# Optimization experiments

Measured on AMD Instinct MI355X. Metric: run time of the kernel, lower is better.

Reference implementation:

```python
import jax, jax.numpy as jnp
import numpy as np

S, N, L, B = 200000, 250000, 64, 64


def setup_inputs() -> dict:
    key = jax.random.key(0)
    k = jax.random.split(key, 7)
    return {
        "We_m": jax.random.normal(k[0], (S, L), jnp.float32) * 0.02,
        "be_m": jax.random.normal(k[1], (L,), jnp.float32) * 0.02,
        "Wd_m": jax.random.normal(k[2], (L, S), jnp.float32) * 0.02,
        "bd_m": jax.random.normal(k[3], (S,), jnp.float32) * 0.02,
        "x": jax.random.normal(k[4], (B, N), jnp.float32),
        "nn_n": jax.random.randint(k[5], (N,), 0, S),  # nearest master node for each new node
        "nn_m": jax.random.randint(k[6], (S,), 0, N),  # nearest new node for each master node
    }


def _reshape_weights(We_m, be_m, Wd_m, bd_m, nn_n, nn_m):
    # Vectorized equivalent of GFN_AE.reshape_weights(expand=True, agglomerate=True,
    # update_master=False, eval mode).
    s, l = We_m.shape
    n = nn_n.shape[0]
    # Expand: new node pt_n is "added" iff nn_m[nn_n[pt_n]] != pt_n.
    added = (nn_m[nn_n] != jnp.arange(n)).astype(We_m.dtype)  # [N]
    # Sequential We_i[pt_m] *= c/(c+1) collapses to division by (c_m + 1),
    # c_m = number of added new nodes whose nearest master node is m.
    c_m = jax.ops.segment_sum(added, nn_n, num_segments=s)  # [S]
    We_s = We_m / (c_m + 1.0)[:, None]  # scaled master encoder rows
    # Appended row i (for added node pt_n, src m = nn_n[pt_n]) equals We_s[m],
    # Wd column / bd entry copied from m; its nn_m_ext entry is pt_n itself.
    # Agglomerate: We_n sums contributors, Wd_n/bd_n take the running mean (= plain mean).
    We_n = jax.ops.segment_sum(We_s, nn_m, num_segments=n) + added[:, None] * We_s[nn_n]
    WdT = Wd_m.T  # [S, L]
    cnt = jax.ops.segment_sum(jnp.ones((s,), We_m.dtype), nn_m, num_segments=n) + added
    denom = jnp.maximum(cnt, 1.0)
    Wd_n = ((jax.ops.segment_sum(WdT, nn_m, num_segments=n) + added[:, None] * WdT[nn_n]) / denom[:, None]).T  # [L, N]
    bd_n = (jax.ops.segment_sum(bd_m, nn_m, num_segments=n) + added * bd_m[nn_n]) / denom  # [N]
    return We_n, Wd_n, bd_n


def reference(We_m, be_m, Wd_m, bd_m, x, nn_n, nn_m):
    We_n, Wd_n, bd_n = _reshape_weights(We_m, be_m, Wd_m, bd_m, nn_n, nn_m)
    z = x @ We_n + be_m            # encode: [B, N] x [N, L]
    out = z @ Wd_n + bd_n          # decode: [B, L] x [L, N]
    return out
```

## Files before the change

### kernel.cpp

```cpp
#include <hip/hip_runtime.h>

constexpr int S_ = 200000;
constexpr int N_ = 250000;

constexpr int NCHUNK = (N_ + 63) / 64;
constexpr int FUSE_BLOCKS = (NCHUNK + 1) / 2;
constexpr int DEC_BLOCKS = NCHUNK;

constexpr int EMASK = 0x3FFFF;

typedef __attribute__((ext_vector_type(8))) short bf16x8;
typedef __attribute__((ext_vector_type(4))) float f32x4;
typedef __attribute__((ext_vector_type(8))) unsigned short us8;

__global__ void k_added_counts(const int* __restrict__ nn_n, const int* __restrict__ nn_m,
                               int* __restrict__ added, int* __restrict__ c_m,
                               int* __restrict__ ecnt) {
    int i = blockIdx.x * 256 + threadIdx.x;
    if (i < N_) {
        int m = nn_n[i];
        int a = (nn_m[m] != i) ? 1 : 0;
        added[i] = a;
        if (a) {
            atomicAdd(&c_m[m], 1);
            atomicAdd(&ecnt[i], 1);
        }
    }
    if (i < S_) {
        atomicAdd(&ecnt[nn_m[i]], 1);
    }
}

__global__ void k_scan_blocksum(const int* __restrict__ ecnt, int* __restrict__ bsum) {
    __shared__ int sd[256];
    int b = blockIdx.x, t = threadIdx.x;
    int base = b * 1024 + t * 4;
    int s = 0;
#pragma unroll
    for (int k = 0; k < 4; k++) { int idx = base + k; if (idx < N_) s += ecnt[idx]; }
    sd[t] = s;
    __syncthreads();
    for (int off = 128; off > 0; off >>= 1) {
        if (t < off) sd[t] += sd[t + off];
        __syncthreads();
    }
    if (t == 0) bsum[b] = sd[0];
}

__global__ void k_scan_apply(const int* __restrict__ ecnt, const int* __restrict__ bsum,
                             int* __restrict__ offs) {
    __shared__ int sd[256];
    __shared__ int sp[256];
    int b = blockIdx.x, t = threadIdx.x;
    sp[t] = (t < b) ? bsum[t] : 0;
    __syncthreads();
    for (int off = 128; off > 0; off >>= 1) {
        if (t < off) sp[t] += sp[t + off];
        __syncthreads();
    }
    int prev = sp[0];

    int base = b * 1024 + t * 4;
    int v[4]; int s = 0;
#pragma unroll
    for (int k = 0; k < 4; k++) { int idx = base + k; v[k] = (idx < N_) ? ecnt[idx] : 0; s += v[k]; }
    sd[t] = s;
    __syncthreads();
    for (int off = 1; off < 256; off <<= 1) {
        int xv = (t >= off) ? sd[t - off] : 0;
        __syncthreads();
        sd[t] += xv;
        __syncthreads();
    }
    int run = prev + sd[t] - s;
#pragma unroll
    for (int k = 0; k < 4; k++) {
        int idx = base + k;
        if (idx < N_) offs[idx] = run;
        run += v[k];
    }
}

__global__ void k_fill(const int* __restrict__ nn_m, const int* __restrict__ nn_n,
                       const int* __restrict__ added, const int* __restrict__ offs,
                       const int* __restrict__ c_m,
                       int* __restrict__ fill, int* __restrict__ elist) {
    int i = blockIdx.x * 256 + threadIdx.x;
    if (i < S_) {
        int j = nn_m[i];
        int p = atomicAdd(&fill[j], 1);
        elist[offs[j] + p] = i | (c_m[i] << 18);
    }
    if (i < N_ && added[i]) {
        int m = nn_n[i];
        int p = atomicAdd(&fill[i], 1);
        elist[offs[i] + p] = m | (c_m[m] << 18);
    }
}

__global__ __launch_bounds__(256) void k_wenc(
        const float* __restrict__ x, const float* __restrict__ We_m,
        const int* __restrict__ ecnt, const int* __restrict__ offs,
        const int* __restrict__ elist, float* __restrict__ zp2) {
    __shared__ unsigned short sw[8192];
    int t = threadIdx.x;
    int lane = t & 63;
    int wv = __builtin_amdgcn_readfirstlane(t >> 6);
    int mrow = lane & 15;
    int kq = lane >> 4;
    int ct = lane >> 4, l15 = lane & 15;
    const float* xbase = x + (size_t)(wv * 16 + mrow) * N_ + kq * 8;
    f32x4 acc[4];
#pragma unroll
    for (int i = 0; i < 4; i++) acc[i] = (f32x4){0.f, 0.f, 0.f, 0.f};

    for (int cc = 0; cc < 2; cc++) {
        int chk = blockIdx.x * 2 + cc;
        if (chk >= NCHUNK) break;
        int n0 = chk * 64;

        __syncthreads();
        int jb = n0 + wv * 16;
        int c[16], o[16];
        float ag[16];
#pragma unroll
        for (int u = 0; u < 16; u++) {
            int j = jb + u;
            bool v = (j < N_);
            c[u] = v ? __builtin_amdgcn_readfirstlane(ecnt[j]) : 0;
            o[u] = v ? __builtin_amdgcn_readfirstlane(offs[j]) : 0;
            ag[u] = 0.f;
        }
        int cmax = 0;
#pragma unroll
        for (int u = 0; u < 16; u++) cmax = max(cmax, c[u]);
        if (cmax > 0) {
            int e[16];
#pragma unroll
            for (int u = 0; u < 16; u++)
                e[u] = __builtin_amdgcn_readfirstlane(elist[o[u]]);
            for (int q = 0; q < cmax; q++) {
                int en[16];
#pragma unroll
                for (int u = 0; u < 16; u++) {
                    int cl = max(c[u] - 1, 0);
                    int p = o[u] + min(q + 1, cl);
                    en[u] = __builtin_amdgcn_readfirstlane(elist[p]);
                }
                float row[16];
#pragma unroll
                for (int u = 0; u < 16; u++) {
                    int mmu = (q < c[u]) ? (e[u] & EMASK) : 0;
                    const float* ap = We_m + (size_t)mmu * 64 + lane;
                    asm volatile("global_load_dword %0, %1, off"
                                 : "=v"(row[u]) : "v"(ap));
                }
                asm volatile("s_waitcnt vmcnt(0)");
                __builtin_amdgcn_sched_barrier(0);
#pragma unroll
                for (int u = 0; u < 16; u++) {
                    float r = __builtin_amdgcn_rcpf((float)((e[u] >> 18) + 1));
                    float sc = (q < c[u]) ? r : 0.0f;
                    ag[u] += row[u] * sc;
                }
#pragma unroll
                for (int u = 0; u < 16; u++) e[u] = en[u];
            }
        }
        us8 h0, l0, h1, l1;
#pragma unroll
        for (int s = 0; s < 8; s++) {
            float v0 = ag[s];
            unsigned u0 = __float_as_uint(v0);
            h0[s] = (unsigned short)(u0 >> 16);
            float r0 = v0 - __uint_as_float(u0 & 0xffff0000u);
            l0[s] = (unsigned short)(__float_as_uint(r0) >> 16);
            float v1 = ag[8 + s];
            unsigned u1 = __float_as_uint(v1);
            h1[s] = (unsigned short)(u1 >> 16);
            float r1 = v1 - __uint_as_float(u1 & 0xffff0000u);
            l1[s] = (unsigned short)(__float_as_uint(r1) >> 16);
        }
        int kq2a = (wv & 1) * 2;
        int sH = wv >> 1;
        int base0 = sH * 4096 + ct * 1024 + (l15 + 16 * kq2a) * 8;
        int base1 = base0 + 128;
        *(us8*)&sw[base0]       = h0;
        *(us8*)&sw[base0 + 512] = l0;
        *(us8*)&sw[base1]       = h1;
        *(us8*)&sw[base1 + 512] = l1;
        __syncthreads();

#pragma unroll
        for (int s = 0; s < 2; s++) {
            float av[8];
            if (n0 + s * 32 + kq * 8 + 8 <= N_) {
                float4 a0 = *(const float4*)(xbase + n0 + s * 32);
                float4 a1 = *(const float4*)(xbase + n0 + s * 32 + 4);
                av[0] = a0.x; av[1] = a0.y; av[2] = a0.z; av[3] = a0.w;
                av[4] = a1.x; av[5] = a1.y; av[6] = a1.z; av[7] = a1.w;
            } else {
#pragma unroll
                for (int i = 0; i < 8; i++) av[i] = 0.f;
            }
            bf16x8 bh[4], bl[4];
#pragma unroll
            for (int c2 = 0; c2 < 4; c2++) {
                bh[c2] = *(const bf16x8*)&sw[s * 4096 + c2 * 1024 + lane * 8];
                bl[c2] = *(const bf16x8*)&sw[s * 4096 + c2 * 1024 + 512 + lane * 8];
            }
            bf16x8 ah, al;
#pragma unroll
            for (int i = 0; i < 8; i++) {
                float v = av[i];
                unsigned u = __float_as_uint(v);
                ah[i] = (short)(u >> 16);
                float r = v - __uint_as_float(u & 0xffff0000u);
                al[i] = (short)(__float_as_uint(r) >> 16);
            }
#pragma unroll
            for (int c2 = 0; c2 < 4; c2++) {
                acc[c2] = __builtin_amdgcn_mfma_f32_16x16x32_bf16(ah, bh[c2], acc[c2], 0, 0, 0);
                acc[c2] = __builtin_amdgcn_mfma_f32_16x16x32_bf16(al, bh[c2], acc[c2], 0, 0, 0);
                acc[c2] = __builtin_amdgcn_mfma_f32_16x16x32_bf16(ah, bl[c2], acc[c2], 0, 0, 0);
            }
        }
    }

    int row = blockIdx.x & 63;
    float* zr = zp2 + row * 4096;
#pragma unroll
    for (int c2 = 0; c2 < 4; c2++) {
#pragma unroll
        for (int r = 0; r < 4; r++) {
            int b = wv * 16 + kq * 4 + r;
            int l = c2 * 16 + mrow;
            atomicAdd(&zr[b * 64 + l], acc[c2][r]);
        }
    }
}

__global__ void k_zred(const float* __restrict__ zp2, const float* __restrict__ be_m,
                       float* __restrict__ z2g) {
    int slot = blockIdx.x * 256 + threadIdx.x;
    float s = 0.f;
    for (int r = 0; r < 64; r++) s += zp2[r * 4096 + slot];
    int b = slot >> 6, l = slot & 63;
    z2g[l * 64 + b] = s + be_m[l];
}

__global__ __launch_bounds__(256) void k_pmat(
        const float* __restrict__ Wd_m, const float* __restrict__ bd_m,
        const float* __restrict__ z2g, float* __restrict__ P) {
    __shared__ float ws[64 * 64];
    int t = threadIdx.x;
    int m0 = blockIdx.x * 64;
#pragma unroll
    for (int r = 0; r < 4; r++) {
        int flat = r * 256 + t;
        int l = flat >> 4;
        int c4 = flat & 15;
        float4 v = *(const float4*)&Wd_m[(size_t)l * S_ + m0 + c4 * 4];
        *(float4*)&ws[l * 64 + c4 * 4] = v;
    }
    __syncthreads();

    int m = t & 63;
    int bg = __builtin_amdgcn_readfirstlane(t >> 6);
    float bd = bd_m[m0 + m];
    float acc[16];
#pragma unroll
    for (int q = 0; q < 16; q++) acc[q] = bd;
    const float* zb = z2g + bg * 16;
#pragma unroll 4
    for (int l = 0; l < 64; l++) {
        float w = ws[l * 64 + m];
        const float* zr = zb + l * 64;
#pragma unroll
        for (int q = 0; q < 16; q++) acc[q] += w * zr[q];
    }

    float4* Pv = (float4*)&P[(size_t)(m0 + m) * 64 + bg * 16];
#pragma unroll
    for (int q4 = 0; q4 < 4; q4++)
        Pv[q4] = make_float4(acc[q4 * 4 + 0], acc[q4 * 4 + 1],
                             acc[q4 * 4 + 2], acc[q4 * 4 + 3]);
}

__global__ __launch_bounds__(256) void k_decode(const float* __restrict__ P,
        const int* __restrict__ ecnt, const int* __restrict__ offs,
        const int* __restrict__ elist, float* __restrict__ out) {
    __shared__ float tile[64][65];
    int t = threadIdx.x;
    int wv = __builtin_amdgcn_readfirstlane(t >> 6);
    int lane = t & 63;
    int j0 = blockIdx.x * 64;
    int jb = j0 + wv * 16;
    int c[16], o[16];
    float acc[16];
#pragma unroll
    for (int u = 0; u < 16; u++) {
        int j = jb + u;
        bool v = (j < N_);
        c[u] = v ? __builtin_amdgcn_readfirstlane(ecnt[j]) : 0;
        o[u] = v ? __builtin_amdgcn_readfirstlane(offs[j]) : 0;
        acc[u] = 0.f;
    }
    int cmax = 0;
#pragma unroll
    for (int u = 0; u < 16; u++) cmax = max(cmax, c[u]);

    if (cmax > 0) {
        int e[16];
#pragma unroll
        for (int u = 0; u < 16; u++)
            e[u] = __builtin_amdgcn_readfirstlane(elist[o[u]]);
        for (int q = 0; q < cmax; q++) {
            int en[16];
#pragma unroll
            for (int u = 0; u < 16; u++) {
                int cl = max(c[u] - 1, 0);
                int p = o[u] + min(q + 1, cl);
                en[u] = __builtin_amdgcn_readfirstlane(elist[p]);
            }
            float row[16];
#pragma unroll
            for (int u = 0; u < 16; u++) {
                int mmu = (q < c[u]) ? (e[u] & EMASK) : 0;
                const float* ap = P + (size_t)mmu * 64 + lane;
                asm volatile("global_load_dword %0, %1, off"
                             : "=v"(row[u]) : "v"(ap));
            }
            asm volatile("s_waitcnt vmcnt(0)");
            __builtin_amdgcn_sched_barrier(0);
#pragma unroll
            for (int u = 0; u < 16; u++)
                acc[u] += (q < c[u]) ? row[u] : 0.0f;
#pragma unroll
            for (int u = 0; u < 16; u++) e[u] = en[u];
        }
    }
#pragma unroll
    for (int u = 0; u < 16; u++) {
        int cc = (c[u] > 1) ? c[u] : 1;
        tile[wv * 16 + u][lane] = acc[u] * (1.0f / (float)cc);
    }
    __syncthreads();
#pragma unroll
    for (int r = 0; r < 16; r++) {
        int b = r * 4 + wv;
        int j = j0 + lane;
        if (j < N_) out[(size_t)b * N_ + j] = tile[lane][b];
    }
}

extern "C" void kernel_launch(void* const* d_in, const int* in_sizes, int n_in,
                              void* d_out, int out_size, void* d_ws, size_t ws_size,
                              hipStream_t stream) {
    const float* We_m = (const float*)d_in[0];
    const float* be_m = (const float*)d_in[1];
    const float* Wd_m = (const float*)d_in[2];
    const float* bd_m = (const float*)d_in[3];
    const float* x    = (const float*)d_in[4];
    const int*   nn_n = (const int*)d_in[5];
    const int*   nn_m = (const int*)d_in[6];
    float* out = (float*)d_out;
    char* ws = (char*)d_ws;

    float* P     = (float*)(ws + 0);
    int*   c_m   = (int*)(ws + 64012288);
    int*   ecnt  = (int*)(ws + 64812288);
    int*   fill  = (int*)(ws + 65812288);
    int*   added = (int*)(ws + 66812288);
    int*   offs  = (int*)(ws + 67812288);
    int*   elist = (int*)(ws + 68812288);
    float* zp2   = (float*)(ws + 70812288);
    float* z2g   = (float*)(ws + 71860864);
    int*   bsum  = (int*)(ws + 71877248);

    hipMemsetAsync(ws + 64012288, 0, 2800000, stream);
    hipMemsetAsync(zp2, 0, 1048576, stream);

    k_added_counts<<<977, 256, 0, stream>>>(nn_n, nn_m, added, c_m, ecnt);
    k_scan_blocksum<<<245, 256, 0, stream>>>(ecnt, bsum);
    k_scan_apply<<<245, 256, 0, stream>>>(ecnt, bsum, offs);
    k_fill<<<977, 256, 0, stream>>>(nn_m, nn_n, added, offs, c_m, fill, elist);
    k_wenc<<<FUSE_BLOCKS, 256, 0, stream>>>(x, We_m, ecnt, offs, elist, zp2);
    k_zred<<<16, 256, 0, stream>>>(zp2, be_m, z2g);
    k_pmat<<<3125, 256, 0, stream>>>(Wd_m, bd_m, z2g, P);
    k_decode<<<DEC_BLOCKS, 256, 0, stream>>>(P, ecnt, offs, elist, out);
}
```

Before: 348.1 us.

## Prefetch x early in fused encoder, stage P writes via LDS, halve decode tile

The fused encoder kernel now issues its x-tile loads with inline asm at the top of each chunk, so they overlap the gather/aggregation phase, and waits on them only before the MFMAs. k_pmat stages its results through padded shared memory so P rows are written with coalesced float4 stores. k_decode handles 32 columns per block with 8 rows per wave instead of 16, doubling the block count, and drops the asm loads in favour of plain loads. The aim is to hide latency and raise occupancy, at the cost of more registers held live in the encoder and more, smaller decode blocks.

```diff
diff --git a/kernel.cpp b/kernel.cpp
--- a/kernel.cpp
+++ b/kernel.cpp
@@ -5,7 +5,7 @@
 
 constexpr int NCHUNK = (N_ + 63) / 64;
 constexpr int FUSE_BLOCKS = (NCHUNK + 1) / 2;
-constexpr int DEC_BLOCKS = NCHUNK;
+constexpr int DEC_BLOCKS = (N_ + 31) / 32;
 
 constexpr int EMASK = 0x3FFFF;
 
@@ -118,8 +118,22 @@
         int chk = blockIdx.x * 2 + cc;
         if (chk >= NCHUNK) break;
         int n0 = chk * 64;
-
-        __syncthreads();
+        bool full = (n0 + 64 <= N_);
+
+        __syncthreads();
+
+        f32x4 xa[4];
+        if (full) {
+            const float* a0 = xbase + n0;
+            const float* a1 = xbase + n0 + 4;
+            const float* a2 = xbase + n0 + 32;
+            const float* a3 = xbase + n0 + 36;
+            asm volatile("global_load_dwordx4 %0, %1, off" : "=v"(xa[0]) : "v"(a0));
+            asm volatile("global_load_dwordx4 %0, %1, off" : "=v"(xa[1]) : "v"(a1));
+            asm volatile("global_load_dwordx4 %0, %1, off" : "=v"(xa[2]) : "v"(a2));
+            asm volatile("global_load_dwordx4 %0, %1, off" : "=v"(xa[3]) : "v"(a3));
+        }
+
         int jb = n0 + wv * 16;
         int c[16], o[16];
         float ag[16];
@@ -191,18 +205,30 @@
         *(us8*)&sw[base1 + 512] = l1;
         __syncthreads();
 
+        float av2[2][8];
+        if (full) {
+            asm volatile("s_waitcnt vmcnt(0)");
+            __builtin_amdgcn_sched_barrier(0);
+#pragma unroll
+            for (int i = 0; i < 4; i++) {
+                av2[0][i]     = xa[0][i];
+                av2[0][4 + i] = xa[1][i];
+                av2[1][i]     = xa[2][i];
+                av2[1][4 + i] = xa[3][i];
+            }
+        } else {
+#pragma unroll
+            for (int s = 0; s < 2; s++) {
+#pragma unroll
+                for (int i = 0; i < 8; i++) av2[s][i] = 0.f;
+                int nb = n0 + s * 32 + kq * 8;
+#pragma unroll
+                for (int i = 0; i < 8; i++)
+                    if (nb + i < N_) av2[s][i] = xbase[n0 + s * 32 + i];
+            }
+        }
 #pragma unroll
         for (int s = 0; s < 2; s++) {
-            float av[8];
-            if (n0 + s * 32 + kq * 8 + 8 <= N_) {
-                float4 a0 = *(const float4*)(xbase + n0 + s * 32);
-                float4 a1 = *(const float4*)(xbase + n0 + s * 32 + 4);
-                av[0] = a0.x; av[1] = a0.y; av[2] = a0.z; av[3] = a0.w;
-                av[4] = a1.x; av[5] = a1.y; av[6] = a1.z; av[7] = a1.w;
-            } else {
-#pragma unroll
-                for (int i = 0; i < 8; i++) av[i] = 0.f;
-            }
             bf16x8 bh[4], bl[4];
 #pragma unroll
             for (int c2 = 0; c2 < 4; c2++) {
@@ -212,7 +238,7 @@
             bf16x8 ah, al;
 #pragma unroll
             for (int i = 0; i < 8; i++) {
-                float v = av[i];
+                float v = av2[s][i];
                 unsigned u = __float_as_uint(v);
                 ah[i] = (short)(u >> 16);
                 float r = v - __uint_as_float(u & 0xffff0000u);
@@ -252,7 +278,7 @@
 __global__ __launch_bounds__(256) void k_pmat(
         const float* __restrict__ Wd_m, const float* __restrict__ bd_m,
         const float* __restrict__ z2g, float* __restrict__ P) {
-    __shared__ float ws[64 * 64];
+    __shared__ float ws[4352];
     int t = threadIdx.x;
     int m0 = blockIdx.x * 64;
 #pragma unroll
@@ -280,77 +306,87 @@
         for (int q = 0; q < 16; q++) acc[q] += w * zr[q];
     }
 
-    float4* Pv = (float4*)&P[(size_t)(m0 + m) * 64 + bg * 16];
+    __syncthreads();
 #pragma unroll
     for (int q4 = 0; q4 < 4; q4++)
-        Pv[q4] = make_float4(acc[q4 * 4 + 0], acc[q4 * 4 + 1],
-                             acc[q4 * 4 + 2], acc[q4 * 4 + 3]);
+        *(float4*)&ws[m * 68 + bg * 16 + q4 * 4] =
+            make_float4(acc[q4 * 4 + 0], acc[q4 * 4 + 1],
+                        acc[q4 * 4 + 2], acc[q4 * 4 + 3]);
+    __syncthreads();
+#pragma unroll
+    for (int rep = 0; rep < 4; rep++) {
+        int flat = rep * 256 + t;
+        int rr = flat >> 4, c4 = flat & 15;
+        *(float4*)&P[(size_t)(m0 + rr) * 64 + c4 * 4] =
+            *(const float4*)&ws[rr * 68 + c4 * 4];
+    }
 }
 
 __global__ __launch_bounds__(256) void k_decode(const float* __restrict__ P,
         const int* __restrict__ ecnt, const int* __restrict__ offs,
         const int* __restrict__ elist, float* __restrict__ out) {
-    __shared__ float tile[64][65];
+    __shared__ float tile[32][65];
     int t = threadIdx.x;
     int wv = __builtin_amdgcn_readfirstlane(t >> 6);
     int lane = t & 63;
-    int j0 = blockIdx.x * 64;
-    int jb = j0 + wv * 16;
-    int c[16], o[16];
-    float acc[16];
-#pragma unroll
-    for (int u = 0; u < 16; u++) {
-        int j = jb + u;
+    int j0 = blockIdx.x * 32;
+    int jb = j0 + wv * 8;
+    int c[8], o[8], cl[8];
+    float acc[8];
+#pragma unroll
+    for (int s = 0; s < 8; s++) {
+        int j = jb + s;
         bool v = (j < N_);
-        c[u] = v ? __builtin_amdgcn_readfirstlane(ecnt[j]) : 0;
-        o[u] = v ? __builtin_amdgcn_readfirstlane(offs[j]) : 0;
-        acc[u] = 0.f;
+        c[s] = v ? __builtin_amdgcn_readfirstlane(ecnt[j]) : 0;
+        o[s] = v ? __builtin_amdgcn_readfirstlane(offs[j]) : 0;
+        cl[s] = max(c[s] - 1, 0);
+        acc[s] = 0.f;
     }
     int cmax = 0;
 #pragma unroll
-    for (int u = 0; u < 16; u++) cmax = max(cmax, c[u]);
+    for (int s = 0; s < 8; s++) cmax = max(cmax, c[s]);
 
     if (cmax > 0) {
-        int e[16];
-#pragma unroll
-        for (int u = 0; u < 16; u++)
-            e[u] = __builtin_amdgcn_readfirstlane(elist[o[u]]);
+        int e[8];
+#pragma unroll
+        for (int s = 0; s < 8; s++)
+            e[s] = __builtin_amdgcn_readfirstlane(elist[o[s]]);
         for (int q = 0; q < cmax; q++) {
-            int en[16];
-#pragma unroll
-            for (int u = 0; u < 16; u++) {
-                int cl = max(c[u] - 1, 0);
-                int p = o[u] + min(q + 1, cl);
-                en[u] = __builtin_amdgcn_readfirstlane(elist[p]);
-            }
-            float row[16];
-#pragma unroll
-            for (int u = 0; u < 16; u++) {
-                int mmu = (q < c[u]) ? (e[u] & EMASK) : 0;
-                const float* ap = P + (size_t)mmu * 64 + lane;
-                asm volatile("global_load_dword %0, %1, off"
-                             : "=v"(row[u]) : "v"(ap));
-            }
-            asm volatile("s_waitcnt vmcnt(0)");
-            __builtin_amdgcn_sched_barrier(0);
-#pragma unroll
-            for (int u = 0; u < 16; u++)
-                acc[u] += (q < c[u]) ? row[u] : 0.0f;
-#pragma unroll
-            for (int u = 0; u < 16; u++) e[u] = en[u];
-        }
-    }
-#pragma unroll
-    for (int u = 0; u < 16; u++) {
-        int cc = (c[u] > 1) ? c[u] : 1;
-        tile[wv * 16 + u][lane] = acc[u] * (1.0f / (float)cc);
-    }
-    __syncthreads();
-#pragma unroll
-    for (int r = 0; r < 16; r++) {
-        int b = r * 4 + wv;
-        int j = j0 + lane;
-        if (j < N_) out[(size_t)b * N_ + j] = tile[lane][b];
+            int en[8];
+#pragma unroll
+            for (int s = 0; s < 8; s++) {
+                int p = o[s] + min(q + 1, cl[s]);
+                en[s] = __builtin_amdgcn_readfirstlane(elist[p]);
+            }
+            int mm[8]; float sc[8];
+#pragma unroll
+            for (int s = 0; s < 8; s++) {
+                bool valid = (q < c[s]);
+                mm[s] = valid ? (e[s] & EMASK) : 0;
+                sc[s] = valid ? 1.0f : 0.0f;
+            }
+            float row[8];
+#pragma unroll
+            for (int s = 0; s < 8; s++)
+                row[s] = P[(size_t)mm[s] * 64 + lane];
+#pragma unroll
+            for (int s = 0; s < 8; s++)
+                acc[s] += row[s] * sc[s];
+#pragma unroll
+            for (int s = 0; s < 8; s++) e[s] = en[s];
+        }
+    }
+#pragma unroll
+    for (int s = 0; s < 8; s++) {
+        int cc = (c[s] > 1) ? c[s] : 1;
+        tile[wv * 8 + s][lane] = acc[s] * (1.0f / (float)cc);
+    }
+    __syncthreads();
+#pragma unroll
+    for (int r = 0; r < 8; r++) {
+        int b = r * 8 + (t >> 5);
+        int j = j0 + (t & 31);
+        if (j < N_) out[(size_t)b * N_ + j] = tile[t & 31][b];
     }
 }
 
```

New measurement: 335.2 us. -3.7%, faster.
